# Kernel tuning notes

Measured on AMD Instinct MI355X. Metric: run time of the kernel, lower is better.

## Reference

```python
import jax, jax.numpy as jnp
import numpy as np

NUM_HEADS = 16
D_K = 8  # == n_qubits


def setup_inputs() -> dict:
    key = jax.random.key(0)
    k1, k2, k3 = jax.random.split(key, 3)
    x = jax.random.normal(k1, (4, 2048, 128), dtype=jnp.float32)
    # trainable RX angles, one per qubit (tq.RX has_params=True)
    theta = jax.random.normal(k2, (D_K,), dtype=jnp.float32)
    # out_proj: Linear(embed_dim, embed_dim, bias=False)
    w_out = jax.random.normal(k3, (128, 128), dtype=jnp.float32) * (1.0 / np.sqrt(128.0))
    return {"x": x, "theta": theta, "w_out": w_out}


def quantum_features(x, theta):
    # x: [b, s, e]. Per head of size d_k: encode RX(x_i), trainable RX(theta_i)
    # (composes to RX(x_i + theta_i)), CNOT ladder [i, i+1], measure PauliZ.
    # Heisenberg picture: Z_w -> Z_0...Z_w, so <Z_w> = prod_{i<=w} cos(x_i + theta_i).
    b, s, e = x.shape
    heads = x.reshape(b, s, NUM_HEADS, D_K)
    return jnp.cumprod(jnp.cos(heads + theta), axis=-1)  # [b, s, h, d_k]


def reference(x, theta, w_out):
    b, s, e = x.shape
    # q == k == v: same shared q_layer applied to the same x three times.
    qkv = quantum_features(x, theta)            # [b, s, h, d_k]
    q = qkv.transpose(0, 2, 1, 3)               # [b, h, s, d_k]
    scores = jnp.einsum('bhqd,bhkd->bhqk', q, q) / np.sqrt(D_K)
    attn = jax.nn.softmax(scores, axis=-1)      # dropout is identity at eval
    out = jnp.einsum('bhqk,bhkd->bhqd', attn, q)
    out = out.transpose(0, 2, 1, 3).reshape(b, s, e)
    return out @ w_out.T
```

## Files before the change

kernel.cpp:

```cpp
#include <hip/hip_runtime.h>

#define BATCH 4
#define SEQ   2048
#define EMB   128
#define NH    16
#define DK    8

#define QSCALE 0.510069726f

typedef _Float16 v4h  __attribute__((ext_vector_type(4)));
typedef _Float16 v8h  __attribute__((ext_vector_type(8)));
typedef __fp16   v2fp __attribute__((ext_vector_type(2)));
typedef float    v4f  __attribute__((ext_vector_type(4)));
typedef float    v16f __attribute__((ext_vector_type(16)));


__launch_bounds__(256, 4)
__global__ void feat_kernel(const float* __restrict__ x,
                            const float* __restrict__ theta,
                            _Float16* __restrict__ F1,
                            _Float16* __restrict__ F2) {
  const int tid = threadIdx.x;
  const int bh  = blockIdx.x >> 3;
  const int s   = ((blockIdx.x & 7) << 8) + tid;
  const int b = bh >> 4, h = bh & 15;

  float th[8];
#pragma unroll
  for (int i = 0; i < 8; ++i) th[i] = theta[i];

  const float* xp = x + ((size_t)b * SEQ + s) * EMB + h * DK;
  const float4 a = *(const float4*)(xp);
  const float4 c = *(const float4*)(xp + 4);
  float r[8];
  r[0] = __cosf(a.x + th[0]);
  r[1] = r[0] * __cosf(a.y + th[1]);
  r[2] = r[1] * __cosf(a.z + th[2]);
  r[3] = r[2] * __cosf(a.w + th[3]);
  r[4] = r[3] * __cosf(c.x + th[4]);
  r[5] = r[4] * __cosf(c.y + th[5]);
  r[6] = r[5] * __cosf(c.z + th[6]);
  r[7] = r[6] * __cosf(c.w + th[7]);

  _Float16 hv[8];
#pragma unroll
  for (int i = 0; i < 8; ++i) hv[i] = (_Float16)r[i];

  union { v4h v[2]; float4 f; } u;
  u.v[0] = (v4h){hv[0], hv[1], hv[2], hv[3]};
  u.v[1] = (v4h){hv[4], hv[5], hv[6], hv[7]};
  *(float4*)(F1 + ((size_t)bh * SEQ + s) * 8) = u.f;

  const int sp = (s & ~15) | (s & 3) | ((s & 4) << 1) | ((s & 8) >> 1);
  _Float16* f2 = F2 + (size_t)bh * 9 * SEQ;
#pragma unroll
  for (int d = 0; d < 8; ++d) f2[(size_t)d * SEQ + sp] = hv[d];
  f2[(size_t)8 * SEQ + s] = (_Float16)1.0f;
}

__launch_bounds__(256, 4)
__global__ void attn_kernel(const _Float16* __restrict__ F1,
                            const _Float16* __restrict__ F2,
                            _Float16* __restrict__ Ah ) {
  const int tid = threadIdx.x;
  const int L   = tid & 63;
  const int ln  = L & 31;
  const int hf  = L >> 5;
  const int wv  = tid >> 6;
  const int bh  = blockIdx.x >> 4;
  const int qt  = (blockIdx.x & 15) * 4 + wv;
  const int qb  = qt * 32;
  const int b = bh >> 4, h = bh & 15;
  const int mrow = (ln < 8) ? ln : 8;

  const _Float16* f1 = F1 + (size_t)bh * SEQ * 8;
  const _Float16* kp = f1 + ln * 8;
  const _Float16* vp = F2 + (size_t)bh * 9 * SEQ + (size_t)mrow * SEQ + hf * 8;

  v8h qf = {0, 0, 0, 0, 0, 0, 0, 0};
  if (hf == 0) {
    const v8h qv = *(const v8h*)(f1 + (size_t)(qb + ln) * 8);
    const _Float16 qs = (_Float16)QSCALE;
    const v8h qsc = {qs, qs, qs, qs, qs, qs, qs, qs};
    qf = qv * qsc;
  }

  v16f acc;
#pragma unroll
  for (int i = 0; i < 16; ++i) acc[i] = 0.f;
  v16f zf;
#pragma unroll
  for (int i = 0; i < 16; ++i) zf[i] = 0.f;

  v8h kf0  = *(const v8h*)kp; kp += 256;
  v8h kf_n = *(const v8h*)kp; kp += 256;
  v8h vt0_c = *(const v8h*)(vp);
  v8h vt1_c = *(const v8h*)(vp + 16); vp += 32;
  v16f s_cur = __builtin_amdgcn_mfma_f32_32x32x16_f16(kf0, qf, zf, 0, 0, 0);

#pragma unroll 4
  for (int kb = 0; kb < 63; ++kb) {
    const v8h kf_f = *(const v8h*)kp; kp += 256;
    const v16f s_next = __builtin_amdgcn_mfma_f32_32x32x16_f16(kf_n, qf, zf, 0, 0, 0);
    const v8h vt0_n = *(const v8h*)(vp);
    const v8h vt1_n = *(const v8h*)(vp + 16); vp += 32;
    union { v2fp p[4]; v8h v; } p0, p1;
#pragma unroll
    for (int i = 0; i < 4; ++i) {
      p0.p[i] = __builtin_amdgcn_cvt_pkrtz(
          __builtin_amdgcn_exp2f(s_cur[2 * i]),
          __builtin_amdgcn_exp2f(s_cur[2 * i + 1]));
    }
    acc = __builtin_amdgcn_mfma_f32_32x32x16_f16(vt0_c, p0.v, acc, 0, 0, 0);
#pragma unroll
    for (int i = 0; i < 4; ++i) {
      p1.p[i] = __builtin_amdgcn_cvt_pkrtz(
          __builtin_amdgcn_exp2f(s_cur[8 + 2 * i]),
          __builtin_amdgcn_exp2f(s_cur[8 + 2 * i + 1]));
    }
    acc = __builtin_amdgcn_mfma_f32_32x32x16_f16(vt1_c, p1.v, acc, 0, 0, 0);
    s_cur = s_next; kf_n = kf_f; vt0_c = vt0_n; vt1_c = vt1_n;
  }
  {
    union { v2fp p[4]; v8h v; } p0, p1;
#pragma unroll
    for (int i = 0; i < 4; ++i) {
      p0.p[i] = __builtin_amdgcn_cvt_pkrtz(
          __builtin_amdgcn_exp2f(s_cur[2 * i]),
          __builtin_amdgcn_exp2f(s_cur[2 * i + 1]));
      p1.p[i] = __builtin_amdgcn_cvt_pkrtz(
          __builtin_amdgcn_exp2f(s_cur[8 + 2 * i]),
          __builtin_amdgcn_exp2f(s_cur[8 + 2 * i + 1]));
    }
    acc = __builtin_amdgcn_mfma_f32_32x32x16_f16(vt0_c, p0.v, acc, 0, 0, 0);
    acc = __builtin_amdgcn_mfma_f32_32x32x16_f16(vt1_c, p1.v, acc, 0, 0, 0);
  }

  {
    const float den = __shfl(acc[4], ln, 64);
    const float inv = 1.0f / den;
    const int qrow = qb + ln;
    v4h o = {(_Float16)(acc[0] * inv), (_Float16)(acc[1] * inv),
             (_Float16)(acc[2] * inv), (_Float16)(acc[3] * inv)};
    *(v4h*)(Ah + ((size_t)b * SEQ + qrow) * EMB + h * DK + hf * 4) = o;
  }
}

__launch_bounds__(256, 4)
__global__ void proj_kernel(const _Float16* __restrict__ Ah,
                            const float* __restrict__ W,
                            float* __restrict__ out) {
  __shared__ __align__(16) _Float16 Ahs[64][136];
  __shared__ __align__(16) _Float16 Whs[64][136];

  const int tid  = threadIdx.x;
  const int L    = tid & 63;
  const int wv   = tid >> 6;
  const int quad = L >> 4;
  const int ln   = L & 15;
  const int rowbase = blockIdx.x * 64;
  const int colbase = blockIdx.y * 64;

#pragma unroll
  for (int it = 0; it < 4; ++it) {
    const int idx = it * 256 + tid;
    const int r  = idx >> 4;
    const int c8 = idx & 15;
    *(uint4*)&Ahs[r][c8 * 8] =
        *(const uint4*)(Ah + (size_t)(rowbase + r) * EMB + c8 * 8);
  }
#pragma unroll
  for (int it = 0; it < 8; ++it) {
    const int idx = it * 256 + tid;
    const int n  = idx >> 5;
    const int c4 = idx & 31;
    const float4 w = *(const float4*)(W + (size_t)(colbase + n) * EMB + c4 * 4);
    v4h wh = {(_Float16)w.x, (_Float16)w.y, (_Float16)w.z, (_Float16)w.w};
    *(v4h*)&Whs[n][c4 * 4] = wh;
  }
  __syncthreads();

  v4f acc[4];
#pragma unroll
  for (int nt = 0; nt < 4; ++nt) acc[nt] = (v4f){0.f, 0.f, 0.f, 0.f};

#pragma unroll
  for (int k8 = 0; k8 < 8; ++k8) {
    const v4h af = *(const v4h*)&Ahs[wv * 16 + ln][k8 * 16 + quad * 4];
#pragma unroll
    for (int nt = 0; nt < 4; ++nt) {
      const v4h bf = *(const v4h*)&Whs[nt * 16 + ln][k8 * 16 + quad * 4];
      acc[nt] = __builtin_amdgcn_mfma_f32_16x16x16f16(af, bf, acc[nt], 0, 0, 0);
    }
  }

#pragma unroll
  for (int nt = 0; nt < 4; ++nt) {
    const int col = colbase + nt * 16 + ln;
#pragma unroll
    for (int r = 0; r < 4; ++r) {
      out[(size_t)(rowbase + wv * 16 + quad * 4 + r) * EMB + col] = acc[nt][r];
    }
  }
}

extern "C" void kernel_launch(void* const* d_in, const int* in_sizes, int n_in,
                              void* d_out, int out_size, void* d_ws, size_t ws_size,
                              hipStream_t stream) {
  const float* x     = (const float*)d_in[0];
  const float* theta = (const float*)d_in[1];
  const float* w_out = (const float*)d_in[2];
  float* out = (float*)d_out;

  _Float16* Ah = (_Float16*)d_ws;
  _Float16* F1 = Ah + (size_t)BATCH * SEQ * EMB;
  _Float16* F2 = F1 + (size_t)64 * SEQ * 8 + 512;

  feat_kernel<<<dim3(512), dim3(256), 0, stream>>>(x, theta, F1, F2);

  attn_kernel<<<dim3(1024), dim3(256), 0, stream>>>(F1, F2, Ah);

  proj_kernel<<<dim3((BATCH * SEQ) / 64, 2), dim3(256), 0, stream>>>(Ah, w_out, out);
}
```

Measured before the change: 100.6 us.

## Split key range across wave pairs and share K/V loads across two query tiles

Each wave now processes two 32-row query tiles against half of the key sequence, reusing each loaded K and V fragment for two score and two PV MFMAs. Partial numerators and denominators from the two key halves are combined through shared memory after a block barrier. This halves the per-query K/V global traffic and adds independent MFMA chains for latency hiding. In exchange it drops the explicit software pipelining of the score MFMA, adds an LDS reduction and a sync, and raises register pressure with two accumulators.

Result: faster. 95.79 us (-4.8%).

```diff
diff --git a/kernel.cpp b/kernel.cpp
--- a/kernel.cpp
+++ b/kernel.cpp
@@ -62,86 +62,89 @@
 __global__ void attn_kernel(const _Float16* __restrict__ F1,
                             const _Float16* __restrict__ F2,
                             _Float16* __restrict__ Ah ) {
+  __shared__ float P[4][2][5][64];
+
   const int tid = threadIdx.x;
   const int L   = tid & 63;
   const int ln  = L & 31;
   const int hf  = L >> 5;
   const int wv  = tid >> 6;
+  const int pr  = wv >> 1;
+  const int kh  = wv & 1;
   const int bh  = blockIdx.x >> 4;
-  const int qt  = (blockIdx.x & 15) * 4 + wv;
-  const int qb  = qt * 32;
+  const int qbase = (blockIdx.x & 15) * 128;
   const int b = bh >> 4, h = bh & 15;
   const int mrow = (ln < 8) ? ln : 8;
 
   const _Float16* f1 = F1 + (size_t)bh * SEQ * 8;
-  const _Float16* kp = f1 + ln * 8;
-  const _Float16* vp = F2 + (size_t)bh * 9 * SEQ + (size_t)mrow * SEQ + hf * 8;
-
-  v8h qf = {0, 0, 0, 0, 0, 0, 0, 0};
+  const _Float16* kp = f1 + (size_t)(kh * 1024 + ln) * 8;
+  const _Float16* vp = F2 + (size_t)bh * 9 * SEQ + (size_t)mrow * SEQ
+                          + kh * 1024 + hf * 8;
+
+  v8h qf0 = {0, 0, 0, 0, 0, 0, 0, 0};
+  v8h qf1 = {0, 0, 0, 0, 0, 0, 0, 0};
   if (hf == 0) {
-    const v8h qv = *(const v8h*)(f1 + (size_t)(qb + ln) * 8);
     const _Float16 qs = (_Float16)QSCALE;
     const v8h qsc = {qs, qs, qs, qs, qs, qs, qs, qs};
-    qf = qv * qsc;
-  }
-
-  v16f acc;
-#pragma unroll
-  for (int i = 0; i < 16; ++i) acc[i] = 0.f;
-  v16f zf;
-#pragma unroll
-  for (int i = 0; i < 16; ++i) zf[i] = 0.f;
-
-  v8h kf0  = *(const v8h*)kp; kp += 256;
-  v8h kf_n = *(const v8h*)kp; kp += 256;
-  v8h vt0_c = *(const v8h*)(vp);
-  v8h vt1_c = *(const v8h*)(vp + 16); vp += 32;
-  v16f s_cur = __builtin_amdgcn_mfma_f32_32x32x16_f16(kf0, qf, zf, 0, 0, 0);
-
+    qf0 = *(const v8h*)(f1 + (size_t)(qbase + pr * 64 + ln) * 8) * qsc;
+    qf1 = *(const v8h*)(f1 + (size_t)(qbase + pr * 64 + 32 + ln) * 8) * qsc;
+  }
+
+  v16f acc0, acc1, zf;
+#pragma unroll
+  for (int i = 0; i < 16; ++i) { acc0[i] = 0.f; acc1[i] = 0.f; zf[i] = 0.f; }
+
+  v8h kf = *(const v8h*)kp; kp += 256;
 #pragma unroll 4
-  for (int kb = 0; kb < 63; ++kb) {
-    const v8h kf_f = *(const v8h*)kp; kp += 256;
-    const v16f s_next = __builtin_amdgcn_mfma_f32_32x32x16_f16(kf_n, qf, zf, 0, 0, 0);
-    const v8h vt0_n = *(const v8h*)(vp);
-    const v8h vt1_n = *(const v8h*)(vp + 16); vp += 32;
-    union { v2fp p[4]; v8h v; } p0, p1;
+  for (int kb = 0; kb < 32; ++kb) {
+    const v8h kf_n = *(const v8h*)kp; kp += 256;
+    const v16f s0 = __builtin_amdgcn_mfma_f32_32x32x16_f16(kf, qf0, zf, 0, 0, 0);
+    const v16f s1 = __builtin_amdgcn_mfma_f32_32x32x16_f16(kf, qf1, zf, 0, 0, 0);
+    const v8h vt0 = *(const v8h*)(vp);
+    const v8h vt1 = *(const v8h*)(vp + 16); vp += 32;
+    union { v2fp p[4]; v8h v; } a0, a1, b0, b1;
 #pragma unroll
     for (int i = 0; i < 4; ++i) {
-      p0.p[i] = __builtin_amdgcn_cvt_pkrtz(
-          __builtin_amdgcn_exp2f(s_cur[2 * i]),
-          __builtin_amdgcn_exp2f(s_cur[2 * i + 1]));
-    }
-    acc = __builtin_amdgcn_mfma_f32_32x32x16_f16(vt0_c, p0.v, acc, 0, 0, 0);
+      a0.p[i] = __builtin_amdgcn_cvt_pkrtz(
+          __builtin_amdgcn_exp2f(s0[2 * i]),
+          __builtin_amdgcn_exp2f(s0[2 * i + 1]));
+      a1.p[i] = __builtin_amdgcn_cvt_pkrtz(
+          __builtin_amdgcn_exp2f(s0[8 + 2 * i]),
+          __builtin_amdgcn_exp2f(s0[8 + 2 * i + 1]));
+    }
+    acc0 = __builtin_amdgcn_mfma_f32_32x32x16_f16(vt0, a0.v, acc0, 0, 0, 0);
+    acc0 = __builtin_amdgcn_mfma_f32_32x32x16_f16(vt1, a1.v, acc0, 0, 0, 0);
 #pragma unroll
     for (int i = 0; i < 4; ++i) {
-      p1.p[i] = __builtin_amdgcn_cvt_pkrtz(
-          __builtin_amdgcn_exp2f(s_cur[8 + 2 * i]),
-          __builtin_amdgcn_exp2f(s_cur[8 + 2 * i + 1]));
-    }
-    acc = __builtin_amdgcn_mfma_f32_32x32x16_f16(vt1_c, p1.v, acc, 0, 0, 0);
-    s_cur = s_next; kf_n = kf_f; vt0_c = vt0_n; vt1_c = vt1_n;
-  }
+      b0.p[i] = __builtin_amdgcn_cvt_pkrtz(
+          __builtin_amdgcn_exp2f(s1[2 * i]),
+          __builtin_amdgcn_exp2f(s1[2 * i + 1]));
+      b1.p[i] = __builtin_amdgcn_cvt_pkrtz(
+          __builtin_amdgcn_exp2f(s1[8 + 2 * i]),
+          __builtin_amdgcn_exp2f(s1[8 + 2 * i + 1]));
+    }
+    acc1 = __builtin_amdgcn_mfma_f32_32x32x16_f16(vt0, b0.v, acc1, 0, 0, 0);
+    acc1 = __builtin_amdgcn_mfma_f32_32x32x16_f16(vt1, b1.v, acc1, 0, 0, 0);
+    kf = kf_n;
+  }
+
+#pragma unroll
+  for (int r = 0; r < 5; ++r) {
+    P[wv][0][r][L] = acc0[r];
+    P[wv][1][r][L] = acc1[r];
+  }
+  __syncthreads();
   {
-    union { v2fp p[4]; v8h v; } p0, p1;
-#pragma unroll
-    for (int i = 0; i < 4; ++i) {
-      p0.p[i] = __builtin_amdgcn_cvt_pkrtz(
-          __builtin_amdgcn_exp2f(s_cur[2 * i]),
-          __builtin_amdgcn_exp2f(s_cur[2 * i + 1]));
-      p1.p[i] = __builtin_amdgcn_cvt_pkrtz(
-          __builtin_amdgcn_exp2f(s_cur[8 + 2 * i]),
-          __builtin_amdgcn_exp2f(s_cur[8 + 2 * i + 1]));
-    }
-    acc = __builtin_amdgcn_mfma_f32_32x32x16_f16(vt0_c, p0.v, acc, 0, 0, 0);
-    acc = __builtin_amdgcn_mfma_f32_32x32x16_f16(vt1_c, p1.v, acc, 0, 0, 0);
-  }
-
-  {
-    const float den = __shfl(acc[4], ln, 64);
+    const int p2 = (wv >> 1) << 1;
+    const int c  = wv & 1;
+    float sum[4];
+#pragma unroll
+    for (int r = 0; r < 4; ++r) sum[r] = P[p2][c][r][L] + P[p2 + 1][c][r][L];
+    const float den = P[p2][c][4][ln] + P[p2 + 1][c][4][ln];
     const float inv = 1.0f / den;
-    const int qrow = qb + ln;
-    v4h o = {(_Float16)(acc[0] * inv), (_Float16)(acc[1] * inv),
-             (_Float16)(acc[2] * inv), (_Float16)(acc[3] * inv)};
+    const int qrow = qbase + wv * 32 + ln;
+    v4h o = {(_Float16)(sum[0] * inv), (_Float16)(sum[1] * inv),
+             (_Float16)(sum[2] * inv), (_Float16)(sum[3] * inv)};
     *(v4h*)(Ah + ((size_t)b * SEQ + qrow) * EMB + h * DK + hf * 4) = o;
   }
 }
```
